# Kernel tuning notes

Hardware: AMD Instinct MI355X
Metric: run time of the kernel (lower is better)

Reference implementation:

```python
import jax, jax.numpy as jnp
import numpy as np

EPS = 1e-8  # matches F.normalize / F.cosine_similarity default eps
RAD2DEG = 180.0 / np.pi


def setup_inputs() -> dict:
    key = jax.random.key(0)
    k1, k2, k3, k4 = jax.random.split(key, 4)
    N, D_IN, C = 2_000_000, 64, 3
    data = jax.random.normal(k1, (N, D_IN), dtype=jnp.float32)
    lab = jax.random.normal(k2, (N, C), dtype=jnp.float32)
    W = jax.random.normal(k3, (D_IN, C), dtype=jnp.float32) * 0.1
    b = jax.random.normal(k4, (C,), dtype=jnp.float32) * 0.1
    return {"data": data, "lab": lab, "W": W, "b": b}


def reference(data, lab, W, b):
    # predictor: Linear(64 -> 3)
    pred = data @ W + b  # [N, 3]
    # F.normalize(pred, dim=1): x / max(||x||, eps)
    pred_n = pred / jnp.maximum(jnp.linalg.norm(pred, axis=1, keepdims=True), EPS)
    # F.cosine_similarity(pred_n, lab, dim=1)
    dot = jnp.sum(pred_n * lab, axis=1)  # [N]
    na = jnp.maximum(jnp.linalg.norm(pred_n, axis=1), EPS)
    nb = jnp.maximum(jnp.linalg.norm(lab, axis=1), EPS)
    cos = dot / (na * nb)
    # acos in degrees, then NaN -> 0 (replaces the per-element Python loop)
    loss2 = jnp.arccos(cos) * RAD2DEG
    return jnp.where(jnp.isnan(loss2), 0.0, loss2)
```

## Files before the change

kernel.cpp:

```cpp
#include <hip/hip_runtime.h>
#include <math.h>

#define EPS 1e-8f
#define RAD2DEG 57.29577951308232f

__global__ __launch_bounds__(256) void cos_loss_kernel(
    const float* __restrict__ data,
    const float* __restrict__ lab,
    const float* __restrict__ W,
    const float* __restrict__ b,
    float* __restrict__ out,
    int N)
{
    const int lane  = threadIdx.x & 15;
    const int group = threadIdx.x >> 4;

    float w[4][3];
#pragma unroll
    for (int j = 0; j < 4; ++j)
#pragma unroll
        for (int c = 0; c < 3; ++c)
            w[j][c] = W[(lane * 4 + j) * 3 + c];
    const float b0 = b[0], b1 = b[1], b2 = b[2];

    const int groups_per_block = blockDim.x >> 4;
    const long long stride = (long long)gridDim.x * groups_per_block;

    for (long long row = (long long)blockIdx.x * groups_per_block + group;
         row < N; row += stride) {

        const float4 v = *(const float4*)(data + row * 64 + lane * 4);

        float p0 = v.x * w[0][0] + v.y * w[1][0] + v.z * w[2][0] + v.w * w[3][0];
        float p1 = v.x * w[0][1] + v.y * w[1][1] + v.z * w[2][1] + v.w * w[3][1];
        float p2 = v.x * w[0][2] + v.y * w[1][2] + v.z * w[2][2] + v.w * w[3][2];

#pragma unroll
        for (int off = 8; off > 0; off >>= 1) {
            p0 += __shfl_down(p0, off, 16);
            p1 += __shfl_down(p1, off, 16);
            p2 += __shfl_down(p2, off, 16);
        }

        if (lane == 0) {
            p0 += b0; p1 += b1; p2 += b2;

            float norm = sqrtf(p0 * p0 + p1 * p1 + p2 * p2);
            float inv  = 1.0f / fmaxf(norm, EPS);
            float q0 = p0 * inv, q1 = p1 * inv, q2 = p2 * inv;

            float l0 = lab[row * 3 + 0];
            float l1 = lab[row * 3 + 1];
            float l2 = lab[row * 3 + 2];

            float dot = q0 * l0 + q1 * l1 + q2 * l2;
            float na  = fmaxf(sqrtf(q0 * q0 + q1 * q1 + q2 * q2), EPS);
            float nb  = fmaxf(sqrtf(l0 * l0 + l1 * l1 + l2 * l2), EPS);

            float cosv = dot / (na * nb);
            cosv = fminf(1.0f, fmaxf(-1.0f, cosv));

            float ang = acosf(cosv) * RAD2DEG;
            if (isnan(ang)) ang = 0.0f;
            out[row] = ang;
        }
    }
}

extern "C" void kernel_launch(void* const* d_in, const int* in_sizes, int n_in,
                              void* d_out, int out_size, void* d_ws, size_t ws_size,
                              hipStream_t stream) {
    const float* data = (const float*)d_in[0];
    const float* lab  = (const float*)d_in[1];
    const float* W    = (const float*)d_in[2];
    const float* b    = (const float*)d_in[3];
    float* out        = (float*)d_out;

    const int N = in_sizes[0] / 64;

    const int block = 256;
    const int rows_per_block = block / 16;
    long long need = ((long long)N + rows_per_block - 1) / rows_per_block;
    int grid = (int)(need < 8192 ? need : 8192);
    if (grid < 1) grid = 1;

    cos_loss_kernel<<<grid, block, 0, stream>>>(data, lab, W, b, out, N);
}
```

Before: 676.6 us.

## Tile rows per block and run epilogue across all threads via shared memory

Each block now processes a 256-row tile: 16-lane groups compute the projections and store them to shared memory. After a barrier, every thread handles one row's normalization, cosine and acos. This replaces the lane-0-only epilogue and makes the label reads and output writes coalesced. The grid-stride loop is replaced by one tile per block, which adds a __syncthreads and shared-memory traffic.

```diff
diff --git a/kernel.cpp b/kernel.cpp
--- a/kernel.cpp
+++ b/kernel.cpp
@@ -3,6 +3,7 @@
 
 #define EPS 1e-8f
 #define RAD2DEG 57.29577951308232f
+#define TILE 256
 
 __global__ __launch_bounds__(256) void cos_loss_kernel(
     const float* __restrict__ data,
@@ -12,8 +13,11 @@
     float* __restrict__ out,
     int N)
 {
-    const int lane  = threadIdx.x & 15;
-    const int group = threadIdx.x >> 4;
+    __shared__ float4 pred_s[TILE];
+
+    const int tid   = threadIdx.x;
+    const int lane  = tid & 15;
+    const int group = tid >> 4;
 
     float w[4][3];
 #pragma unroll
@@ -21,15 +25,18 @@
 #pragma unroll
         for (int c = 0; c < 3; ++c)
             w[j][c] = W[(lane * 4 + j) * 3 + c];
-    const float b0 = b[0], b1 = b[1], b2 = b[2];
 
-    const int groups_per_block = blockDim.x >> 4;
-    const long long stride = (long long)gridDim.x * groups_per_block;
+    const int tileBase = blockIdx.x * TILE;
+    const bool full = (tileBase + TILE <= N);
 
-    for (long long row = (long long)blockIdx.x * groups_per_block + group;
-         row < N; row += stride) {
+#pragma unroll 4
+    for (int j = 0; j < 16; ++j) {
+        const int rlocal = j * 16 + group;
+        const int row    = tileBase + rlocal;
 
-        const float4 v = *(const float4*)(data + row * 64 + lane * 4);
+        float4 v = make_float4(0.f, 0.f, 0.f, 0.f);
+        if (full || row < N)
+            v = *(const float4*)(data + (size_t)row * 64 + lane * 4);
 
         float p0 = v.x * w[0][0] + v.y * w[1][0] + v.z * w[2][0] + v.w * w[3][0];
         float p1 = v.x * w[0][1] + v.y * w[1][1] + v.z * w[2][1] + v.w * w[3][1];
@@ -42,28 +49,37 @@
             p2 += __shfl_down(p2, off, 16);
         }
 
-        if (lane == 0) {
-            p0 += b0; p1 += b1; p2 += b2;
+        if (lane == 0)
+            pred_s[rlocal] = make_float4(p0, p1, p2, 0.f);
+    }
 
-            float norm = sqrtf(p0 * p0 + p1 * p1 + p2 * p2);
-            float inv  = 1.0f / fmaxf(norm, EPS);
-            float q0 = p0 * inv, q1 = p1 * inv, q2 = p2 * inv;
+    __syncthreads();
 
-            float l0 = lab[row * 3 + 0];
-            float l1 = lab[row * 3 + 1];
-            float l2 = lab[row * 3 + 2];
+    const int row = tileBase + tid;
+    if (row < N) {
+        const float4 p = pred_s[tid];
+        float p0 = p.x + b[0];
+        float p1 = p.y + b[1];
+        float p2 = p.z + b[2];
 
-            float dot = q0 * l0 + q1 * l1 + q2 * l2;
-            float na  = fmaxf(sqrtf(q0 * q0 + q1 * q1 + q2 * q2), EPS);
-            float nb  = fmaxf(sqrtf(l0 * l0 + l1 * l1 + l2 * l2), EPS);
+        float norm = sqrtf(p0 * p0 + p1 * p1 + p2 * p2);
+        float inv  = 1.0f / fmaxf(norm, EPS);
+        float q0 = p0 * inv, q1 = p1 * inv, q2 = p2 * inv;
 
-            float cosv = dot / (na * nb);
-            cosv = fminf(1.0f, fmaxf(-1.0f, cosv));
+        const float l0 = lab[row * 3 + 0];
+        const float l1 = lab[row * 3 + 1];
+        const float l2 = lab[row * 3 + 2];
 
-            float ang = acosf(cosv) * RAD2DEG;
-            if (isnan(ang)) ang = 0.0f;
-            out[row] = ang;
-        }
+        float dot = q0 * l0 + q1 * l1 + q2 * l2;
+        float na  = fmaxf(sqrtf(q0 * q0 + q1 * q1 + q2 * q2), EPS);
+        float nb  = fmaxf(sqrtf(l0 * l0 + l1 * l1 + l2 * l2), EPS);
+
+        float cosv = dot / (na * nb);
+        cosv = fminf(1.0f, fmaxf(-1.0f, cosv));
+
+        float ang = acosf(cosv) * RAD2DEG;
+        if (isnan(ang)) ang = 0.0f;
+        out[row] = ang;
     }
 }
 
@@ -78,11 +94,6 @@
 
     const int N = in_sizes[0] / 64;
 
-    const int block = 256;
-    const int rows_per_block = block / 16;
-    long long need = ((long long)N + rows_per_block - 1) / rows_per_block;
-    int grid = (int)(need < 8192 ? need : 8192);
-    if (grid < 1) grid = 1;
-
-    cos_loss_kernel<<<grid, block, 0, stream>>>(data, lab, W, b, out, N);
+    const int grid = (N + TILE - 1) / TILE;
+    cos_loss_kernel<<<grid, 256, 0, stream>>>(data, lab, W, b, out, N);
 }
```

After: 671.6 us. No clear change (-0.7%).
